# Kernel optimization log

Hardware: AMD Instinct MI355X
Metric: run time of the kernel (lower is better)

Reference implementation:

```python
import jax, jax.numpy as jnp
import numpy as np

N_WIRES = 10
N_OPS = 30
C64 = jnp.complex64

# Frozen random circuit (stand-in for tq.RandomLayer(n_ops=30)): deterministic op list.
_rng = np.random.default_rng(42)
OPS = []
for _ in range(N_OPS):
    k = int(_rng.integers(0, 4))
    if k == 3:
        w = _rng.choice(N_WIRES, size=2, replace=False)
        OPS.append(('cnot', int(w[0]), int(w[1])))
    else:
        OPS.append((('rx', 'ry', 'rz')[k], int(_rng.integers(0, N_WIRES)), -1))


def _rx_mat(t):
    c = jnp.cos(t / 2).astype(C64)
    s = jnp.sin(t / 2).astype(C64)
    return jnp.stack([jnp.stack([c, -1j * s]), jnp.stack([-1j * s, c])])


def _ry_mat(t):
    c = jnp.cos(t / 2).astype(C64)
    s = jnp.sin(t / 2).astype(C64)
    return jnp.stack([jnp.stack([c, -s]), jnp.stack([s, c])])


def _rz_mat(t):
    tc = t.astype(C64)
    z = jnp.zeros((), C64)
    return jnp.stack([jnp.stack([jnp.exp(-1j * tc / 2), z]), jnp.stack([z, jnp.exp(1j * tc / 2)])])

_GATE = {'rx': _rx_mat, 'ry': _ry_mat, 'rz': _rz_mat}


def _apply_1q(state, U, w):
    # state: [bsz] + [2]*N_WIRES ; apply 2x2 U on qubit axis w
    s = jnp.moveaxis(state, 1 + w, -1)
    s = jnp.einsum('ij,...j->...i', U, s)
    return jnp.moveaxis(s, -1, 1 + w)


def _apply_cnot(state, c, t):
    s = jnp.moveaxis(state, (1 + c, 1 + t), (-2, -1))
    s = jnp.stack([s[..., 0, :], s[..., 1, ::-1]], axis=-2)  # flip target when control=1
    return jnp.moveaxis(s, (-2, -1), (1 + c, 1 + t))


def _quantum_head(x, rand_params, rx_theta, ry_theta, head_w, head_b):
    bsz = x.shape[0]
    # GeneralEncoder '10xRy': RY(x[:,w])|0> per wire -> product state built directly
    state = jnp.ones((bsz, 1), C64)
    for w in range(N_WIRES):
        vec = jnp.stack([jnp.cos(x[:, w] / 2), jnp.sin(x[:, w] / 2)], axis=-1).astype(C64)
        state = (state[:, :, None] * vec[:, None, :]).reshape(bsz, -1)
    state = state.reshape((bsz,) + (2,) * N_WIRES)
    # RandomLayer (frozen 30-op circuit, one angle per op)
    for i, (kind, a, b) in enumerate(OPS):
        if kind == 'cnot':
            state = _apply_cnot(state, a, b)
        else:
            state = _apply_1q(state, _GATE[kind](rand_params[i]), a)
    # shared trainable RX then RY applied to every wire (single shared param each)
    Urx = _rx_mat(rx_theta[0])
    Ury = _ry_mat(ry_theta[0])
    for w in range(N_WIRES):
        state = _apply_1q(state, Urx, w)
        state = _apply_1q(state, Ury, w)
    # MeasureAll(PauliZ): <Z_w> = P(bit_w=0) - P(bit_w=1)
    probs = jnp.abs(state) ** 2  # float32, [bsz] + [2]*n
    feats = []
    for w in range(N_WIRES):
        axes = tuple(1 + q for q in range(N_WIRES) if q != w)
        p = probs.sum(axis=axes)  # [bsz, 2]
        feats.append(p[:, 0] - p[:, 1])
    feats = jnp.stack(feats, axis=-1)  # [bsz, n_wires]
    return feats @ head_w + head_b[0]


def _mlp(x, w0, b0, w1, b1, w2, b2, w3, b3):
    # faithful to ClassicalMLP: Linear chain with NO activations
    h = x @ w0.T + b0
    h = h @ w1.T + b1
    h = h @ w2.T + b2
    return (h @ w3.T + b3)[:, 0]


def setup_inputs() -> dict:
    key = jax.random.key(0)
    ks = jax.random.split(key, 14)
    BSZ = 8192
    return {
        'state_batch': jax.random.normal(ks[0], (BSZ, N_WIRES), jnp.float32),
        'rand_params': jax.random.normal(ks[1], (N_OPS,), jnp.float32),
        'rx_theta': jax.random.normal(ks[2], (1,), jnp.float32),
        'ry_theta': jax.random.normal(ks[3], (1,), jnp.float32),
        'head_w': jax.random.normal(ks[4], (N_WIRES,), jnp.float32) * 0.3,
        'head_b': jax.random.normal(ks[5], (1,), jnp.float32) * 0.1,
        'w0': jax.random.normal(ks[6], (64, N_WIRES), jnp.float32) * 0.3,
        'b0': jax.random.normal(ks[7], (64,), jnp.float32) * 0.1,
        'w1': jax.random.normal(ks[8], (32, 64), jnp.float32) * 0.12,
        'b1': jax.random.normal(ks[9], (32,), jnp.float32) * 0.1,
        'w2': jax.random.normal(ks[10], (16, 32), jnp.float32) * 0.17,
        'b2': jax.random.normal(ks[11], (16,), jnp.float32) * 0.1,
        'w3': jax.random.normal(ks[12], (1, 16), jnp.float32) * 0.25,
        'b3': jax.random.normal(ks[13], (1,), jnp.float32) * 0.1,
    }


def reference(state_batch, rand_params, rx_theta, ry_theta, head_w, head_b, w0, b0, w1, b1, w2, b2, w3, b3):
    q = _quantum_head(state_batch, rand_params, rx_theta, ry_theta, head_w, head_b)
    c = _mlp(state_batch, w0, b0, w1, b1, w2, b2, w3, b3)
    return q + c
```

## Files before the change

kernel.cpp:

```cpp
#include <hip/hip_runtime.h>
#include <cstdint>

#define NW 10
#define NOPS 30

namespace {

typedef unsigned __int128 u128;

struct CRng { u128 state; u128 inc; bool has32; uint32_t cached; };

constexpr u128 PCG_MUL = (((u128)0x2360ED051FC65DA4ULL) << 64) | (u128)0x4385DF649FCCF645ULL;

constexpr void cr_step(CRng &r) { r.state = r.state * PCG_MUL + r.inc; }

constexpr uint64_t cr_out(u128 st) {
  uint64_t hi = (uint64_t)(st >> 64);
  uint64_t lo = (uint64_t)st;
  unsigned rot = (unsigned)(st >> 122) & 63u;
  uint64_t v = hi ^ lo;
  return (v >> rot) | (v << ((64u - rot) & 63u));
}

constexpr uint64_t cr_next64(CRng &r) { cr_step(r); return cr_out(r.state); }

constexpr uint32_t cr_next32(CRng &r) {
  if (r.has32) { r.has32 = false; return r.cached; }
  uint64_t v = cr_next64(r);
  r.has32 = true; r.cached = (uint32_t)(v >> 32);
  return (uint32_t)v;
}

constexpr CRng cr_seed(uint32_t ent) {
  uint32_t pool[4] = {0u, 0u, 0u, 0u};
  uint32_t hc = 0x43b0d7e5u;
  for (int i = 0; i < 4; i++) {
    uint32_t v = (i == 0) ? ent : 0u;
    v ^= hc; hc *= 0x931e8875u; v *= hc; v ^= v >> 16;
    pool[i] = v;
  }
  for (int s = 0; s < 4; s++)
    for (int d = 0; d < 4; d++)
      if (s != d) {
        uint32_t v = pool[s];
        v ^= hc; hc *= 0x931e8875u; v *= hc; v ^= v >> 16;
        uint32_t res = 0xca01f9ddu * pool[d] - 0x4973f715u * v;
        res ^= res >> 16;
        pool[d] = res;
      }
  uint32_t hb = 0x8b51f9ddu;
  uint64_t s64[4] = {0ull, 0ull, 0ull, 0ull};
  for (int i = 0; i < 8; i++) {
    uint32_t d = pool[i & 3];
    d ^= hb; hb *= 0x58f38dedu; d *= hb; d ^= d >> 16;
    if (i & 1) s64[i >> 1] |= ((uint64_t)d << 32); else s64[i >> 1] = (uint64_t)d;
  }
  CRng r{};
  u128 initstate = (((u128)s64[0]) << 64) | (u128)s64[1];
  u128 initseq   = (((u128)s64[2]) << 64) | (u128)s64[3];
  r.state = 0; r.inc = (initseq << 1) | (u128)1;
  cr_step(r);
  r.state += initstate;
  cr_step(r);
  r.has32 = false; r.cached = 0u;
  return r;
}

constexpr uint32_t cr_lemire32(CRng &r, uint32_t rng) {
  uint32_t rng_excl = rng + 1u;
  uint64_t m = (uint64_t)cr_next32(r) * (uint64_t)rng_excl;
  uint32_t leftover = (uint32_t)m;
  if (leftover < rng_excl) {
    uint32_t threshold = (uint32_t)(0xFFFFFFFFu - rng) % rng_excl;
    while (leftover < threshold) {
      m = (uint64_t)cr_next32(r) * (uint64_t)rng_excl;
      leftover = (uint32_t)m;
    }
  }
  return (uint32_t)(m >> 32);
}

constexpr bool canary_pcg42() {
  CRng r = cr_seed(42u);
  double a = (double)(cr_next64(r) >> 11) * (1.0 / 9007199254740992.0);
  double b = (double)(cr_next64(r) >> 11) * (1.0 / 9007199254740992.0);
  double c = (double)(cr_next64(r) >> 11) * (1.0 / 9007199254740992.0);
  bool ok = (a > 0.77395603) && (a < 0.77395607);
  ok = ok && (b > 0.43887842) && (b < 0.43887846);
  ok = ok && (c > 0.85859790) && (c < 0.85859794);
  return ok;
}
static_assert(canary_pcg42(), "CANARY_PCG_SEED42_RANDOM_MISMATCH");

struct COp { int kind; int a; int b; int slot; };
struct Circ { COp op[NOPS]; };

constexpr Circ build_circuit() {
  Circ c{};
  CRng r = cr_seed(42u);
  for (int i = 0; i < NOPS; i++) {
    int k = (int)cr_lemire32(r, 3u);
    if (k == 3) {
      uint32_t v8 = cr_lemire32(r, 8u);
      uint32_t v9 = cr_lemire32(r, 9u);
      uint32_t i0 = v8;
      uint32_t i1 = (v9 == v8) ? 9u : v9;
      uint32_t j = cr_lemire32(r, 1u);
      if (j == 0u) { uint32_t t = i0; i0 = i1; i1 = t; }
      c.op[i] = COp{3, (int)i0, (int)i1, i};
    } else {
      int w = (int)cr_lemire32(r, 9u);
      c.op[i] = COp{k, w, 0, i};
    }
  }
  return c;
}
constexpr Circ CC = build_circuit();

constexpr int MAXP = 16384;
constexpr int MAXU = 4096;

struct Tables {
  int np, nu, overflow;
  uint32_t pmeta[MAXP]; uint32_t pcm[MAXP]; uint32_t psm[MAXP];
  uint32_t ukey[MAXU];  int ustart[MAXU + 1];
};

constexpr Tables build_tables() {
  Tables T{};
  uint32_t meta[MAXP] = {}; uint32_t cm[MAXP] = {}; uint32_t sm[MAXP] = {};
  int np = 0; int ovf = 0;
  for (int w = 0; w < NW; w++)
    for (int src = 0; src < 3; src++) {
      uint32_t xm = (src != 0) ? (1u << w) : 0u;
      uint32_t zm = (src != 1) ? (1u << w) : 0u;
      meta[np] = xm | (zm << 10) | ((uint32_t)w << 21) | ((uint32_t)src << 25);
      cm[np] = 0u; sm[np] = 0u; np++;
    }
  for (int k = NOPS - 1; k >= 0 && !ovf; k--) {
    const COp op = CC.op[k];
    if (op.kind == 3) {
      const int c = op.a, t = op.b;
      for (int p = 0; p < np; p++) {
        uint32_t m = meta[p];
        uint32_t xm = m & 1023u, zm = (m >> 10) & 1023u;
        uint32_t xc = (xm >> c) & 1u, zc = (zm >> c) & 1u;
        uint32_t xt = (xm >> t) & 1u, zt = (zm >> t) & 1u;
        uint32_t fl = xc & zt & (1u ^ (xt ^ zc));
        xm ^= xc << t;
        zm ^= zt << c;
        m = (m & ~(1023u | (1023u << 10))) | xm | (zm << 10);
        m ^= fl << 20;
        meta[p] = m;
      }
    } else {
      const int q = op.a, ax = op.kind, bit = op.slot;
      const int n0 = np;
      for (int p = 0; p < n0; p++) {
        uint32_t m = meta[p];
        uint32_t x = (m >> q) & 1u;
        uint32_t z = (m >> (10 + q)) & 1u;
        uint32_t viol = (ax == 0) ? z : (ax == 1) ? (x ^ z) : x;
        if (viol) {
          uint32_t nx = 0, nz = 0, fl = 0;
          if (ax == 0)      { if (x) { nx = 0; nz = 1; fl = 1; } else { nx = 1; nz = 1; fl = 0; } }
          else if (ax == 1) { if (x) { nx = 0; nz = 1; fl = 0; } else { nx = 1; nz = 0; fl = 1; } }
          else              { if (z) { nx = 1; nz = 0; fl = 0; } else { nx = 1; nz = 1; fl = 1; } }
          if (np >= MAXP) { ovf = 1; break; }
          uint32_t m2 = m;
          m2 &= ~((1u << q) | (1u << (10 + q)));
          m2 |= (nx << q) | (nz << (10 + q));
          m2 ^= fl << 20;
          meta[np] = m2; cm[np] = cm[p]; sm[np] = sm[p] | (1u << bit);
          np++;
          cm[p] |= 1u << bit;
        }
      }
    }
  }
  if (ovf) { T.overflow = 1; return T; }
  int n2 = 0;
  for (int p = 0; p < np; p++) {
    uint32_t m = meta[p];
    if ((m & 1023u) & ((m >> 10) & 1023u)) continue;
    meta[n2] = m; cm[n2] = cm[p]; sm[n2] = sm[p]; n2++;
  }
  np = n2;
  int idx[MAXP] = {}; int tmp[MAXP] = {};
  for (int i = 0; i < np; i++) idx[i] = i;
  int hist[1025] = {};
  for (int i = 0; i < 1025; i++) hist[i] = 0;
  for (int i = 0; i < np; i++) hist[1 + (meta[idx[i]] & 1023u)]++;
  for (int i = 0; i < 1024; i++) hist[i + 1] += hist[i];
  for (int i = 0; i < np; i++) tmp[hist[meta[idx[i]] & 1023u]++] = idx[i];
  for (int i = 0; i < 1025; i++) hist[i] = 0;
  for (int i = 0; i < np; i++) hist[1 + ((meta[tmp[i]] >> 10) & 1023u)]++;
  for (int i = 0; i < 1024; i++) hist[i + 1] += hist[i];
  for (int i = 0; i < np; i++) idx[hist[(meta[tmp[i]] >> 10) & 1023u]++] = tmp[i];
  int nu = 0; uint32_t prev = 0xFFFFFFFFu;
  for (int i = 0; i < np; i++) {
    int p = idx[i];
    uint32_t key = meta[p] & 0xFFFFFu;
    if (key != prev) {
      if (nu >= MAXU) { T.overflow = 2; return T; }
      T.ukey[nu] = key; T.ustart[nu] = i; prev = key; nu++;
    }
    T.pmeta[i] = meta[p]; T.pcm[i] = cm[p]; T.psm[i] = sm[p];
  }
  T.ustart[nu] = np;
  T.np = np; T.nu = nu; T.overflow = 0;
  return T;
}

constexpr Tables TT = build_tables();
static_assert(TT.overflow == 0, "PAULI_PATH_OVERFLOW_raise_MAXP_or_pivot_to_runtime_tables");
static_assert(TT.nu >= 1 && TT.nu <= MAXU, "PAULI_UNIQUE_COUNT_OUT_OF_RANGE");
constexpr int NU = TT.nu;

}

__device__ const Tables dTT = TT;

__global__ __launch_bounds__(256) void prep_kernel(
    const float* __restrict__ rand_params,
    const float* __restrict__ rx_theta, const float* __restrict__ ry_theta,
    const float* __restrict__ head_w, const float* __restrict__ head_b,
    const float* __restrict__ w0, const float* __restrict__ b0,
    const float* __restrict__ w1, const float* __restrict__ b1,
    const float* __restrict__ w2, const float* __restrict__ b2,
    const float* __restrict__ w3, const float* __restrict__ b3,
    float* __restrict__ ws)
{
  const int tid = threadIdx.x;
  __shared__ float ct[32], st[32], abr[3], hwsh[10];
  __shared__ float r2[32], r1[64];

  if (tid < NOPS) {
    float t = rand_params[tid];
    ct[tid] = cosf(t);
    st[tid] = sinf(t);
  }
  if (tid == 30) {
    float tx = rx_theta[0], ty = ry_theta[0];
    abr[0] = cosf(tx) * cosf(ty);
    abr[1] = -sinf(ty);
    abr[2] = sinf(tx) * cosf(ty);
  }
  if (tid < NW) hwsh[tid] = head_w[tid];
  __syncthreads();

  for (int u = tid; u < NU; u += 256) {
    float acc = 0.f;
    const int i0 = dTT.ustart[u], i1 = dTT.ustart[u + 1];
    for (int i = i0; i < i1; i++) {
      uint32_t m = dTT.pmeta[i];
      float v = hwsh[(m >> 21) & 15u] * abr[(m >> 25) & 3u];
      if (m & (1u << 20)) v = -v;
      uint32_t c = dTT.pcm[i];
      while (c) { int b = __builtin_ctz(c); v *= ct[b]; c &= c - 1u; }
      uint32_t s = dTT.psm[i];
      while (s) { int b = __builtin_ctz(s); v *= st[b]; s &= s - 1u; }
      acc += v;
    }
    ws[u] = acc;
  }

  if (tid < 32) {
    float acc = 0.f;
    for (int k = 0; k < 16; k++) acc += w3[k] * w2[k*32 + tid];
    r2[tid] = acc;
  }
  __syncthreads();
  if (tid < 64) {
    float acc = 0.f;
    for (int k = 0; k < 32; k++) acc += r2[k] * w1[k*64 + tid];
    r1[tid] = acc;
  }
  __syncthreads();
  if (tid < NW) {
    float acc = 0.f;
    for (int k = 0; k < 64; k++) acc += r1[k] * w0[k*NW + tid];
    ws[NU + tid] = acc;
  }
  if (tid == NW) {
    float acc = b3[0] + head_b[0];
    for (int k = 0; k < 16; k++) acc += w3[k] * b2[k];
    for (int k = 0; k < 32; k++) acc += r2[k] * b1[k];
    for (int k = 0; k < 64; k++) acc += r1[k] * b0[k];
    ws[NU + NW] = acc;
  }
}

__global__ __launch_bounds__(256) void qsim_kernel(
    const float* __restrict__ x,
    const float* __restrict__ ws,
    float* __restrict__ out,
    int bsz)
{
  __shared__ float    Csh[NU];
  __shared__ uint32_t Ksh[NU];
  const int tid = threadIdx.x;
  for (int i = tid; i < NU; i += 256) {
    Csh[i] = ws[i];
    Ksh[i] = dTT.ukey[i];
  }
  __syncthreads();

  const int wv = (int)((blockIdx.x * blockDim.x + tid) >> 6);
  const int lane = tid & 63;
  if (wv >= bsz) return;
  const float* xe = x + wv * NW;

  float cz[NW], sx[NW];
#pragma unroll
  for (int w = 0; w < NW; w++) {
    float xv = xe[w];
    cz[w] = __cosf(xv);
    sx[w] = __sinf(xv);
  }

  float acc = 0.f;
  for (int s = lane; s < NU; s += 64) {
    uint32_t k = Ksh[s];
    float v = Csh[s];
#pragma unroll
    for (int w = 0; w < NW; w++) {
      float f = ((k >> w) & 1u) ? sx[w]
              : (((k >> (10 + w)) & 1u) ? cz[w] : 1.0f);
      v *= f;
    }
    acc += v;
  }

#pragma unroll
  for (int m = 1; m < 64; m <<= 1) acc += __shfl_xor(acc, m);

  if (lane == 0) {
    float cc = ws[NU + NW];
#pragma unroll
    for (int w = 0; w < NW; w++) cc += xe[w] * ws[NU + w];
    out[wv] = acc + cc;
  }
}

extern "C" void kernel_launch(void* const* d_in, const int* in_sizes, int n_in,
                              void* d_out, int out_size, void* d_ws, size_t ws_size,
                              hipStream_t stream) {
  const float* x   = (const float*)d_in[0];
  const float* rp  = (const float*)d_in[1];
  const float* rxT = (const float*)d_in[2];
  const float* ryT = (const float*)d_in[3];
  const float* hw  = (const float*)d_in[4];
  const float* hb  = (const float*)d_in[5];
  const float* w0  = (const float*)d_in[6];
  const float* b0  = (const float*)d_in[7];
  const float* w1  = (const float*)d_in[8];
  const float* b1  = (const float*)d_in[9];
  const float* w2  = (const float*)d_in[10];
  const float* b2  = (const float*)d_in[11];
  const float* w3  = (const float*)d_in[12];
  const float* b3  = (const float*)d_in[13];
  const int bsz = in_sizes[0] / NW;

  float* ws = (float*)d_ws;

  hipLaunchKernelGGL(prep_kernel, dim3(1), dim3(256), 0, stream,
                     rp, rxT, ryT, hw, hb, w0, b0, w1, b1, w2, b2, w3, b3, ws);

  const int blocks = (bsz + 3) / 4;
  hipLaunchKernelGGL(qsim_kernel, dim3(blocks), dim3(256), 0, stream,
                     x, ws, (float*)d_out, bsz);
}
```

Baseline: 93.28 us.

## Use base-3 half-register lookup tables and prune near-zero Pauli coefficients

Each Pauli key is encoded as two base-3 indices over 5 wires. Per batch element, the wavefront builds two 243-entry product tables in shared memory, so each term becomes two lookups and a multiply instead of a 10-factor select chain. The prep kernel also compacts the term list, dropping coefficients with magnitude at or below 1e-6 via a shared atomic counter. Compaction shrinks the work, but it makes term order nondeterministic and drops small terms, which can change the result slightly. The per-wavefront table build also adds a cost.

Result: slower. 99.21 us (+6.4%).

```diff
diff --git a/kernel.cpp b/kernel.cpp
--- a/kernel.cpp
+++ b/kernel.cpp
@@ -3,6 +3,8 @@
 
 #define NW 10
 #define NOPS 30
+
+typedef float v2fp __attribute__((ext_vector_type(2)));
 
 namespace {
 
@@ -123,7 +125,7 @@
 struct Tables {
   int np, nu, overflow;
   uint32_t pmeta[MAXP]; uint32_t pcm[MAXP]; uint32_t psm[MAXP];
-  uint32_t ukey[MAXU];  int ustart[MAXU + 1];
+  uint32_t upack[MAXU]; int ustart[MAXU + 1];
 };
 
 constexpr Tables build_tables() {
@@ -197,13 +199,24 @@
   for (int i = 0; i < np; i++) hist[1 + ((meta[tmp[i]] >> 10) & 1023u)]++;
   for (int i = 0; i < 1024; i++) hist[i + 1] += hist[i];
   for (int i = 0; i < np; i++) idx[hist[(meta[tmp[i]] >> 10) & 1023u]++] = tmp[i];
+  constexpr int P3[5] = {1, 3, 9, 27, 81};
   int nu = 0; uint32_t prev = 0xFFFFFFFFu;
   for (int i = 0; i < np; i++) {
     int p = idx[i];
     uint32_t key = meta[p] & 0xFFFFFu;
     if (key != prev) {
       if (nu >= MAXU) { T.overflow = 2; return T; }
-      T.ukey[nu] = key; T.ustart[nu] = i; prev = key; nu++;
+      uint32_t tlo = 0, thi = 0;
+      for (int w = 0; w < 5; w++) {
+        uint32_t d = ((key >> w) & 1u) ? 1u : (((key >> (10 + w)) & 1u) ? 2u : 0u);
+        tlo += d * (uint32_t)P3[w];
+      }
+      for (int w = 5; w < 10; w++) {
+        uint32_t d = ((key >> w) & 1u) ? 1u : (((key >> (10 + w)) & 1u) ? 2u : 0u);
+        thi += d * (uint32_t)P3[w - 5];
+      }
+      T.upack[nu] = tlo | (thi << 8);
+      T.ustart[nu] = i; prev = key; nu++;
     }
     T.pmeta[i] = meta[p]; T.pcm[i] = cm[p]; T.psm[i] = sm[p];
   }
@@ -213,9 +226,12 @@
 }
 
 constexpr Tables TT = build_tables();
-static_assert(TT.overflow == 0, "PAULI_PATH_OVERFLOW_raise_MAXP_or_pivot_to_runtime_tables");
+static_assert(TT.overflow == 0, "PAULI_PATH_OVERFLOW");
 static_assert(TT.nu >= 1 && TT.nu <= MAXU, "PAULI_UNIQUE_COUNT_OUT_OF_RANGE");
 constexpr int NU = TT.nu;
+
+constexpr int PAIRS_OFF = 16;
+constexpr int WOFF = PAIRS_OFF + 2 * NU;
 
 }
 
@@ -234,7 +250,9 @@
   const int tid = threadIdx.x;
   __shared__ float ct[32], st[32], abr[3], hwsh[10];
   __shared__ float r2[32], r1[64];
-
+  __shared__ int lcnt;
+
+  if (tid == 0) lcnt = 0;
   if (tid < NOPS) {
     float t = rand_params[tid];
     ct[tid] = cosf(t);
@@ -249,6 +267,7 @@
   if (tid < NW) hwsh[tid] = head_w[tid];
   __syncthreads();
 
+  v2fp* pairs = (v2fp*)(ws + PAIRS_OFF);
   for (int u = tid; u < NU; u += 256) {
     float acc = 0.f;
     const int i0 = dTT.ustart[u], i1 = dTT.ustart[u + 1];
@@ -262,8 +281,16 @@
       while (s) { int b = __builtin_ctz(s); v *= st[b]; s &= s - 1u; }
       acc += v;
     }
-    ws[u] = acc;
-  }
+    if (fabsf(acc) > 1e-6f) {
+      int id = atomicAdd(&lcnt, 1);
+      v2fp p;
+      p.x = acc;
+      p.y = __uint_as_float(dTT.upack[u]);
+      pairs[id] = p;
+    }
+  }
+  __syncthreads();
+  if (tid == 0) ((int*)ws)[0] = lcnt;
 
   if (tid < 32) {
     float acc = 0.f;
@@ -280,14 +307,14 @@
   if (tid < NW) {
     float acc = 0.f;
     for (int k = 0; k < 64; k++) acc += r1[k] * w0[k*NW + tid];
-    ws[NU + tid] = acc;
+    ws[WOFF + tid] = acc;
   }
   if (tid == NW) {
     float acc = b3[0] + head_b[0];
     for (int k = 0; k < 16; k++) acc += w3[k] * b2[k];
     for (int k = 0; k < 32; k++) acc += r2[k] * b1[k];
     for (int k = 0; k < 64; k++) acc += r1[k] * b0[k];
-    ws[NU + NW] = acc;
+    ws[WOFF + NW] = acc;
   }
 }
 
@@ -297,17 +324,20 @@
     float* __restrict__ out,
     int bsz)
 {
-  __shared__ float    Csh[NU];
-  __shared__ uint32_t Ksh[NU];
+  __shared__ v2fp  Psh[NU];
+  __shared__ float Tlo[4][256];
+  __shared__ float Thi[4][256];
+
   const int tid = threadIdx.x;
-  for (int i = tid; i < NU; i += 256) {
-    Csh[i] = ws[i];
-    Ksh[i] = dTT.ukey[i];
-  }
+  const int nu_eff = ((const int*)ws)[0];
+
+  const v2fp* pairs = (const v2fp*)(ws + PAIRS_OFF);
+  for (int i = tid; i < nu_eff; i += 256) Psh[i] = pairs[i];
   __syncthreads();
 
   const int wv = (int)((blockIdx.x * blockDim.x + tid) >> 6);
   const int lane = tid & 63;
+  const int e = tid >> 6;
   if (wv >= bsz) return;
   const float* xe = x + wv * NW;
 
@@ -319,26 +349,33 @@
     sx[w] = __sinf(xv);
   }
 
+  for (int t = lane; t < 243; t += 64) {
+    float vlo = 1.f, vhi = 1.f;
+    int q = t;
+#pragma unroll
+    for (int w = 0; w < 5; w++) {
+      int d = q % 3; q /= 3;
+      vlo *= (d == 1) ? sx[w]     : ((d == 2) ? cz[w]     : 1.0f);
+      vhi *= (d == 1) ? sx[w + 5] : ((d == 2) ? cz[w + 5] : 1.0f);
+    }
+    Tlo[e][t] = vlo;
+    Thi[e][t] = vhi;
+  }
+
   float acc = 0.f;
-  for (int s = lane; s < NU; s += 64) {
-    uint32_t k = Ksh[s];
-    float v = Csh[s];
-#pragma unroll
-    for (int w = 0; w < NW; w++) {
-      float f = ((k >> w) & 1u) ? sx[w]
-              : (((k >> (10 + w)) & 1u) ? cz[w] : 1.0f);
-      v *= f;
-    }
-    acc += v;
+  for (int i = lane; i < nu_eff; i += 64) {
+    v2fp pr = Psh[i];
+    uint32_t pk = __float_as_uint(pr.y);
+    acc += pr.x * Tlo[e][pk & 255u] * Thi[e][pk >> 8];
   }
 
 #pragma unroll
   for (int m = 1; m < 64; m <<= 1) acc += __shfl_xor(acc, m);
 
   if (lane == 0) {
-    float cc = ws[NU + NW];
+    float cc = ws[WOFF + NW];
 #pragma unroll
-    for (int w = 0; w < NW; w++) cc += xe[w] * ws[NU + w];
+    for (int w = 0; w < NW; w++) cc += xe[w] * ws[WOFF + w];
     out[wv] = acc + cc;
   }
 }
```
